# Performance work log

Measured on AMD Instinct MI355X. Metric: run time of the kernel, lower is better.

## Reference

```python
import jax, jax.numpy as jnp
import numpy as np

N = 10000   # nodes
E = 50000   # edges
C = 64      # in_channels / hidden
OUT = 64    # final out_channels


def _conv(x, src, dst, edge_attr, nn_w, nn_b, lin_w, bias):
    # edge MLP -> per-edge weight matrix [E, C, C]
    W = (edge_attr @ nn_w + nn_b).reshape(-1, C, C)
    x_j = x[src]                                   # gather source features [E, C]
    msg = jnp.einsum('ei,eio->eo', x_j, W)         # batched matvec [E, C]
    out = jax.ops.segment_sum(msg, dst, num_segments=N)  # scatter-add to targets
    out = out + x @ lin_w + bias                   # root weight + bias
    return out


def setup_inputs() -> dict:
    key = jax.random.key(0)
    ks = jax.random.split(key, 13)
    s = 1.0 / np.sqrt(C).astype(np.float32)
    return {
        'feature': jax.random.normal(ks[0], (N, C), dtype=jnp.float32),
        'edge_index': jax.random.randint(ks[1], (2, E), 0, N),
        'edge_attr': jax.random.normal(ks[2], (E, C), dtype=jnp.float32),
        # conv layer 0 (in=64 -> out=64)
        'nn_w0': jax.random.normal(ks[3], (C, C * C), dtype=jnp.float32) * s,
        'nn_b0': jnp.zeros((C * C,), dtype=jnp.float32),
        'lin_w0': jax.random.normal(ks[4], (C, C), dtype=jnp.float32) * s,
        'bias0': jnp.zeros((C,), dtype=jnp.float32),
        # conv layer 1 (64 -> 64)
        'nn_w1': jax.random.normal(ks[5], (C, C * C), dtype=jnp.float32) * s,
        'nn_b1': jnp.zeros((C * C,), dtype=jnp.float32),
        'lin_w1': jax.random.normal(ks[6], (C, C), dtype=jnp.float32) * s,
        'bias1': jnp.zeros((C,), dtype=jnp.float32),
        # final linear 64 -> 64
        'fin_w': jax.random.normal(ks[7], (C, OUT), dtype=jnp.float32) * s,
        'fin_b': jnp.zeros((OUT,), dtype=jnp.float32),
    }


def reference(feature, edge_index, edge_attr,
              nn_w0, nn_b0, lin_w0, bias0,
              nn_w1, nn_b1, lin_w1, bias1,
              fin_w, fin_b):
    src, dst = edge_index[0], edge_index[1]  # PyG flow: source_to_target
    x = jax.nn.relu(_conv(feature, src, dst, edge_attr, nn_w0, nn_b0, lin_w0, bias0))
    x = jax.nn.relu(_conv(x, src, dst, edge_attr, nn_w1, nn_b1, lin_w1, bias1))
    return x @ fin_w + fin_b
```

## Files before the change

### kernel.cpp

```cpp
#include <hip/hip_runtime.h>


#define NNODES 10000
#define NEDGES 50000
#define CH 64
#define NSTAGES 65
#define MW 64

typedef _Float16 f16;
typedef f16 f16x8 __attribute__((ext_vector_type(8)));
typedef float f32x4 __attribute__((ext_vector_type(4)));


__global__ void zero_kernel(int* __restrict__ hist, int* __restrict__ cursor) {
    int idx = blockIdx.x * 256 + threadIdx.x;
    if (idx < NNODES) { hist[idx] = 0; cursor[idx] = 0; }
}

__global__ void hist_kernel(const int* __restrict__ ei, int* __restrict__ hist) {
    int e = blockIdx.x * 256 + threadIdx.x;
    if (e < NEDGES) atomicAdd(&hist[ei[NEDGES + e]], 1);
}

__global__ __launch_bounds__(1024)
void scan_kernel(const int* __restrict__ hist, int* __restrict__ start) {
    __shared__ int buf[1024];
    int t = threadIdx.x;
    int base = t * 10;
    int loc[10];
    int s = 0;
#pragma unroll
    for (int i = 0; i < 10; ++i) {
        int n = base + i;
        int v = (n < NNODES) ? hist[n] : 0;
        loc[i] = s; s += v;
    }
    buf[t] = s;
    __syncthreads();
    for (int off = 1; off < 1024; off <<= 1) {
        int add = (t >= off) ? buf[t - off] : 0;
        __syncthreads();
        buf[t] += add;
        __syncthreads();
    }
    int ebase = buf[t] - s;
#pragma unroll
    for (int i = 0; i < 10; ++i) {
        int n = base + i;
        if (n < NNODES) start[n] = ebase + loc[i];
    }
    if (t == 1023) start[NNODES] = buf[1023];
}

__global__ void perm_kernel(const int* __restrict__ ei,
                            const int* __restrict__ start,
                            int* __restrict__ cursor,
                            int* __restrict__ eperm,
                            int* __restrict__ esrc) {
    int e = blockIdx.x * 256 + threadIdx.x;
    if (e < NEDGES) {
        int d = ei[NEDGES + e];
        int pos = start[d] + atomicAdd(&cursor[d], 1);
        eperm[pos] = e;
        esrc[pos]  = ei[e];
    }
}

__global__ void eagather_kernel(const float* __restrict__ ea,
                                const int* __restrict__ eperm,
                                float* __restrict__ eas) {
    int idx = blockIdx.x * 256 + threadIdx.x;
    if (idx >= NEDGES * 16) return;
    int p = idx >> 4, quad = idx & 15;
    int e = eperm[p];
    *(float4*)(eas + (size_t)p * 64 + quad * 4) =
        *(const float4*)(ea + (size_t)e * 64 + quad * 4);
}

__global__ void pack_b_kernel(const float* __restrict__ nw0, const float* __restrict__ nb0,
                              const float* __restrict__ nw1, const float* __restrict__ nb1,
                              f16* __restrict__ Bp0, f16* __restrict__ Bp1) {
    int idx = blockIdx.x * 256 + threadIdx.x;
    if (idx >= 2 * NSTAGES * 2048) return;
    int layer = (idx >= NSTAGES * 2048) ? 1 : 0;
    int r = idx - layer * NSTAGES * 2048;
    const float* nn_w = layer ? nw1 : nw0;
    const float* nn_b = layer ? nb1 : nb0;
    f16* Bp = layer ? Bp1 : Bp0;
    int p  = r & 3;
    int f  = r >> 2;
    int ln = f & 63;
    int q2 = (f >> 6) & 7;
    int s  = f >> 9;
    int tn = q2 >> 1, h = q2 & 1;
    int col  = tn * 16 + (ln & 15);
    int koff = h * 32 + (ln >> 4) * 8 + p * 2;
    float v0, v1;
    if (s < 64) {
        v0 = nn_w[(size_t)koff * 4096 + s * 64 + col];
        v1 = nn_w[(size_t)(koff + 1) * 4096 + s * 64 + col];
    } else {
        v0 = nn_b[koff * 64 + col];
        v1 = nn_b[(koff + 1) * 64 + col];
    }
    union { f16 h2[2]; unsigned u; } pk;
    pk.h2[0] = (f16)v0; pk.h2[1] = (f16)v1;
    *(unsigned*)((char*)Bp + (size_t)f * 16 + p * 4) = pk.u;
}

template<bool RELU_IN>
__global__ __launch_bounds__(64, 2)
void edge_gemm_kernel(const float* __restrict__ x,
                      const int* __restrict__ esrc,
                      const float* __restrict__ eas,
                      const f16* __restrict__ Bp,
                      float* __restrict__ msg) {
    __shared__ f16 xjS[MW][72];

    int ln  = threadIdx.x;
    int l15 = ln & 15, l4 = ln >> 4;
    int e0  = blockIdx.x * MW;
    int nh  = blockIdx.y;

#pragma unroll
    for (int r = 0; r < 16; ++r) {
        int idx = r * 64 + ln;
        int el = idx >> 4, ip = idx & 15;
        int p  = e0 + el;
        float4 v = {0.f, 0.f, 0.f, 0.f};
        if (p < NEDGES)
            v = *(const float4*)(x + (size_t)esrc[p] * CH + ip * 4);
        if (RELU_IN) {
            v.x = fmaxf(v.x, 0.f); v.y = fmaxf(v.y, 0.f);
            v.z = fmaxf(v.z, 0.f); v.w = fmaxf(v.w, 0.f);
        }
        union { f16 h4[4]; uint2 u; } pk;
        pk.h4[0] = (f16)v.x; pk.h4[1] = (f16)v.y;
        pk.h4[2] = (f16)v.z; pk.h4[3] = (f16)v.w;
        *(uint2*)&xjS[el][ip * 4] = pk.u;
    }

    f16x8 eav[4][2];
#pragma unroll
    for (int ms = 0; ms < 4; ++ms) {
        int p = e0 + ms * 16 + l15;
#pragma unroll
        for (int h = 0; h < 2; ++h) {
            float4 a = {0.f,0.f,0.f,0.f}, b = {0.f,0.f,0.f,0.f};
            if (p < NEDGES) {
                const float4* q = (const float4*)(eas + (size_t)p * CH + h * 32 + l4 * 8);
                a = q[0]; b = q[1];
            }
            f16x8 f;
            f[0]=(f16)a.x; f[1]=(f16)a.y; f[2]=(f16)a.z; f[3]=(f16)a.w;
            f[4]=(f16)b.x; f[5]=(f16)b.y; f[6]=(f16)b.z; f[7]=(f16)b.w;
            eav[ms][h] = f;
        }
    }

    f32x4 acc[4][2];
#pragma unroll
    for (int ms = 0; ms < 4; ++ms)
#pragma unroll
        for (int tl = 0; tl < 2; ++tl)
            acc[ms][tl] = (f32x4){0.f, 0.f, 0.f, 0.f};

    const char* gB = (const char*)Bp + nh * 4096 + ln * 16;

#define LOADB(b, sidx) do {                                                     \
        const char* _p = gB + (size_t)(sidx) * 8192;                            \
        b[0] = *(const f16x8*)(_p);                                             \
        b[1] = *(const f16x8*)(_p + 1024);                                      \
        b[2] = *(const f16x8*)(_p + 2048);                                      \
        b[3] = *(const f16x8*)(_p + 3072);                                      \
    } while (0)

#define COMP(sidx, b) do {                                                      \
        _Pragma("unroll")                                                       \
        for (int ms = 0; ms < 4; ++ms) {                                        \
            f16 xv = xjS[ms * 16 + l15][(sidx)];                                \
            f16x8 xsp = {xv, xv, xv, xv, xv, xv, xv, xv};                       \
            f16x8 a0 = eav[ms][0] * xsp;                                        \
            f16x8 a1 = eav[ms][1] * xsp;                                        \
            _Pragma("unroll")                                                   \
            for (int tl = 0; tl < 2; ++tl) {                                    \
                acc[ms][tl] = __builtin_amdgcn_mfma_f32_16x16x32_f16(a0, b[tl*2+0], acc[ms][tl], 0, 0, 0); \
                acc[ms][tl] = __builtin_amdgcn_mfma_f32_16x16x32_f16(a1, b[tl*2+1], acc[ms][tl], 0, 0, 0); \
            }                                                                   \
        }                                                                       \
    } while (0)

#define WAIT8 do { asm volatile("s_waitcnt vmcnt(8)" ::: "memory");             \
                   __builtin_amdgcn_sched_barrier(0); } while (0)

    f16x8 b0[4], b1[4], b2[4];
    LOADB(b0, 0); LOADB(b1, 1); LOADB(b2, 2);
    asm volatile("s_waitcnt vmcnt(0)" ::: "memory");
    __builtin_amdgcn_sched_barrier(0);

#pragma unroll 1
    for (int s = 0; s < 63; s += 3) {
        WAIT8; COMP(s,     b0); LOADB(b0, s + 3);
        WAIT8; COMP(s + 1, b1); LOADB(b1, s + 4);
        WAIT8; COMP(s + 2, b2); LOADB(b2, min(s + 5, 64));
    }
    WAIT8;
    COMP(63, b0);
    asm volatile("s_waitcnt vmcnt(4)" ::: "memory");
    __builtin_amdgcn_sched_barrier(0);
#pragma unroll
    for (int ms = 0; ms < 4; ++ms)
#pragma unroll
        for (int h = 0; h < 2; ++h) {
            f16x8 af = *(const f16x8*)&xjS[ms * 16 + l15][h * 32 + l4 * 8];
#pragma unroll
            for (int tl = 0; tl < 2; ++tl)
                acc[ms][tl] = __builtin_amdgcn_mfma_f32_16x16x32_f16(af, b1[tl * 2 + h], acc[ms][tl], 0, 0, 0);
        }

#pragma unroll
    for (int ms = 0; ms < 4; ++ms)
#pragma unroll
        for (int q = 0; q < 4; ++q) {
            int p = e0 + ms * 16 + l4 * 4 + q;
            if (p < NEDGES) {
                float* row = msg + (size_t)p * CH + nh * 32;
                row[l15]      = acc[ms][0][q];
                row[16 + l15] = acc[ms][1][q];
            }
        }
#undef LOADB
#undef COMP
#undef WAIT8
}

template<bool RELU_IN>
__global__ __launch_bounds__(256)
void rootreduce_kernel(const float* __restrict__ x,
                       const float* __restrict__ lw,
                       const float* __restrict__ bias,
                       const float* __restrict__ msg,
                       const int* __restrict__ start,
                       float* __restrict__ outb) {
    int o  = threadIdx.x & 63;
    int gw = (blockIdx.x * 256 + threadIdx.x) >> 6;
    float lwc[64];
#pragma unroll
    for (int k = 0; k < 64; ++k) lwc[k] = lw[k * 64 + o];
    float bo = bias[o];
    for (int n = gw; n < NNODES; n += 1024) {
        const float4* xr = (const float4*)(x + (size_t)n * 64);
        float acc = bo;
#pragma unroll
        for (int kq = 0; kq < 16; ++kq) {
            float4 xv = xr[kq];
            float a = xv.x, b = xv.y, c = xv.z, d = xv.w;
            if (RELU_IN) {
                a = fmaxf(a, 0.f); b = fmaxf(b, 0.f);
                c = fmaxf(c, 0.f); d = fmaxf(d, 0.f);
            }
            acc = fmaf(a, lwc[kq * 4 + 0], acc);
            acc = fmaf(b, lwc[kq * 4 + 1], acc);
            acc = fmaf(c, lwc[kq * 4 + 2], acc);
            acc = fmaf(d, lwc[kq * 4 + 3], acc);
        }
        int pb = start[n], pe = start[n + 1];
        int p = pb;
        for (; p + 4 <= pe; p += 4) {
            float v0 = msg[(size_t)(p + 0) * 64 + o];
            float v1 = msg[(size_t)(p + 1) * 64 + o];
            float v2 = msg[(size_t)(p + 2) * 64 + o];
            float v3 = msg[(size_t)(p + 3) * 64 + o];
            acc += (v0 + v1) + (v2 + v3);
        }
        for (; p < pe; ++p)
            acc += msg[(size_t)p * 64 + o];
        outb[(size_t)n * 64 + o] = acc;
    }
}

__global__ __launch_bounds__(256)
void final_kernel(const float* __restrict__ x,
                  const float* __restrict__ fw,
                  const float* __restrict__ fb,
                  float* __restrict__ out) {
    int o  = threadIdx.x & 63;
    int gw = (blockIdx.x * 256 + threadIdx.x) >> 6;
    float fwc[64];
#pragma unroll
    for (int k = 0; k < 64; ++k) fwc[k] = fw[k * 64 + o];
    float bo = fb[o];
    for (int n = gw; n < NNODES; n += 1024) {
        const float4* xr = (const float4*)(x + (size_t)n * 64);
        float acc = bo;
#pragma unroll
        for (int kq = 0; kq < 16; ++kq) {
            float4 xv = xr[kq];
            acc = fmaf(fmaxf(xv.x, 0.f), fwc[kq * 4 + 0], acc);
            acc = fmaf(fmaxf(xv.y, 0.f), fwc[kq * 4 + 1], acc);
            acc = fmaf(fmaxf(xv.z, 0.f), fwc[kq * 4 + 2], acc);
            acc = fmaf(fmaxf(xv.w, 0.f), fwc[kq * 4 + 3], acc);
        }
        out[(size_t)n * 64 + o] = acc;
    }
}

extern "C" void kernel_launch(void* const* d_in, const int* in_sizes, int n_in,
                              void* d_out, int out_size, void* d_ws, size_t ws_size,
                              hipStream_t stream) {
    const float* feature = (const float*)d_in[0];
    const int*   ei      = (const int*)d_in[1];
    const float* ea      = (const float*)d_in[2];
    const float* nn_w0   = (const float*)d_in[3];
    const float* nn_b0   = (const float*)d_in[4];
    const float* lin_w0  = (const float*)d_in[5];
    const float* bias0   = (const float*)d_in[6];
    const float* nn_w1   = (const float*)d_in[7];
    const float* nn_b1   = (const float*)d_in[8];
    const float* lin_w1  = (const float*)d_in[9];
    const float* bias1   = (const float*)d_in[10];
    const float* fin_w   = (const float*)d_in[11];
    const float* fin_b   = (const float*)d_in[12];
    float* out = (float*)d_out;

    char* ws = (char*)d_ws;
    float* buf0   = (float*)(ws + 0);
    float* buf1   = (float*)(ws + 2560000);
    f16*   Bp0    = (f16*)  (ws + 5120000);
    f16*   Bp1    = (f16*)  (ws + 5652480);
    int*   hist   = (int*)  (ws + 6184960);
    int*   cursor = (int*)  (ws + 6224960);
    int*   startp = (int*)  (ws + 6264960);
    int*   eperm  = (int*)  (ws + 6304976);
    int*   esrc   = (int*)  (ws + 6504976);
    float* eas    = (float*)(ws + 6704976);
    float* msg    = (float*)(ws + 19504976);

    zero_kernel<<<(NNODES + 255) / 256, 256, 0, stream>>>(hist, cursor);
    hist_kernel<<<(NEDGES + 255) / 256, 256, 0, stream>>>(ei, hist);
    scan_kernel<<<1, 1024, 0, stream>>>(hist, startp);
    perm_kernel<<<(NEDGES + 255) / 256, 256, 0, stream>>>(ei, startp, cursor, eperm, esrc);
    eagather_kernel<<<(NEDGES * 16 + 255) / 256, 256, 0, stream>>>(ea, eperm, eas);

    pack_b_kernel<<<(2 * NSTAGES * 2048 + 255) / 256, 256, 0, stream>>>(
        nn_w0, nn_b0, nn_w1, nn_b1, Bp0, Bp1);

    dim3 eg((NEDGES + MW - 1) / MW, 2);

    edge_gemm_kernel<false><<<eg, 64, 0, stream>>>(feature, esrc, eas, Bp0, msg);
    rootreduce_kernel<false><<<256, 256, 0, stream>>>(feature, lin_w0, bias0,
                                                      msg, startp, buf0);
    edge_gemm_kernel<true><<<eg, 64, 0, stream>>>(buf0, esrc, eas, Bp1, msg);
    rootreduce_kernel<true><<<256, 256, 0, stream>>>(buf0, lin_w1, bias1,
                                                     msg, startp, buf1);
    final_kernel<<<256, 256, 0, stream>>>(buf1, fin_w, fin_b, out);
}
```

Before: 174.6 us.

## Stage B tiles through LDS with async global_load_lds ring and fuse final linear

The edge GEMM now streams the packed per-edge weight tiles into a 6-deep LDS ring using global_load_lds instead of holding triple-buffered register copies, and drops the 2-waves-per-SIMD launch bound. The final linear layer is fused into the second root/reduce kernel through a per-wave shared row, which removes one launch and one intermediate buffer round trip. The zero kernel is replaced by memset calls. The LDS ring adds about 24KB of shared memory per block, which may lower occupancy. The LDS reads in COMP rely only on vmcnt waits with no barrier, which is safe only because each block is a single wave.

```diff
diff --git a/kernel.cpp b/kernel.cpp
--- a/kernel.cpp
+++ b/kernel.cpp
@@ -11,11 +11,10 @@
 typedef f16 f16x8 __attribute__((ext_vector_type(8)));
 typedef float f32x4 __attribute__((ext_vector_type(4)));
 
-
-__global__ void zero_kernel(int* __restrict__ hist, int* __restrict__ cursor) {
-    int idx = blockIdx.x * 256 + threadIdx.x;
-    if (idx < NNODES) { hist[idx] = 0; cursor[idx] = 0; }
-}
+#define GLOAD_LDS16(gptr, lptr) __builtin_amdgcn_global_load_lds(               \
+        (const __attribute__((address_space(1))) void*)(gptr),                  \
+        (__attribute__((address_space(3))) void*)(lptr), 16, 0, 0)
+
 
 __global__ void hist_kernel(const int* __restrict__ ei, int* __restrict__ hist) {
     int e = blockIdx.x * 256 + threadIdx.x;
@@ -109,13 +108,14 @@
 }
 
 template<bool RELU_IN>
-__global__ __launch_bounds__(64, 2)
+__global__ __launch_bounds__(64)
 void edge_gemm_kernel(const float* __restrict__ x,
                       const int* __restrict__ esrc,
                       const float* __restrict__ eas,
                       const f16* __restrict__ Bp,
                       float* __restrict__ msg) {
     __shared__ f16 xjS[MW][72];
+    __shared__ __align__(16) f16 BS[6][2048];
 
     int ln  = threadIdx.x;
     int l15 = ln & 15, l4 = ln >> 4;
@@ -167,56 +167,69 @@
 
     const char* gB = (const char*)Bp + nh * 4096 + ln * 16;
 
-#define LOADB(b, sidx) do {                                                     \
-        const char* _p = gB + (size_t)(sidx) * 8192;                            \
-        b[0] = *(const f16x8*)(_p);                                             \
-        b[1] = *(const f16x8*)(_p + 1024);                                      \
-        b[2] = *(const f16x8*)(_p + 2048);                                      \
-        b[3] = *(const f16x8*)(_p + 3072);                                      \
+#define STAGE(ring, sidx) do {                                                  \
+        const char* _g = gB + (size_t)(sidx) * 8192;                            \
+        char* _l = (char*)&BS[(ring)][0];                                       \
+        GLOAD_LDS16(_g,        _l);                                             \
+        GLOAD_LDS16(_g + 1024, _l + 1024);                                      \
+        GLOAD_LDS16(_g + 2048, _l + 2048);                                      \
+        GLOAD_LDS16(_g + 3072, _l + 3072);                                      \
     } while (0)
 
-#define COMP(sidx, b) do {                                                      \
+#define COMP(sidx, ring) do {                                                   \
+        f16x8 bf0 = *(const f16x8*)&BS[(ring)][ln * 8];                         \
+        f16x8 bf1 = *(const f16x8*)&BS[(ring)][512 + ln * 8];                   \
+        f16x8 bf2 = *(const f16x8*)&BS[(ring)][1024 + ln * 8];                  \
+        f16x8 bf3 = *(const f16x8*)&BS[(ring)][1536 + ln * 8];                  \
         _Pragma("unroll")                                                       \
         for (int ms = 0; ms < 4; ++ms) {                                        \
             f16 xv = xjS[ms * 16 + l15][(sidx)];                                \
             f16x8 xsp = {xv, xv, xv, xv, xv, xv, xv, xv};                       \
             f16x8 a0 = eav[ms][0] * xsp;                                        \
             f16x8 a1 = eav[ms][1] * xsp;                                        \
-            _Pragma("unroll")                                                   \
-            for (int tl = 0; tl < 2; ++tl) {                                    \
-                acc[ms][tl] = __builtin_amdgcn_mfma_f32_16x16x32_f16(a0, b[tl*2+0], acc[ms][tl], 0, 0, 0); \
-                acc[ms][tl] = __builtin_amdgcn_mfma_f32_16x16x32_f16(a1, b[tl*2+1], acc[ms][tl], 0, 0, 0); \
-            }                                                                   \
+            acc[ms][0] = __builtin_amdgcn_mfma_f32_16x16x32_f16(a0, bf0, acc[ms][0], 0, 0, 0); \
+            acc[ms][0] = __builtin_amdgcn_mfma_f32_16x16x32_f16(a1, bf1, acc[ms][0], 0, 0, 0); \
+            acc[ms][1] = __builtin_amdgcn_mfma_f32_16x16x32_f16(a0, bf2, acc[ms][1], 0, 0, 0); \
+            acc[ms][1] = __builtin_amdgcn_mfma_f32_16x16x32_f16(a1, bf3, acc[ms][1], 0, 0, 0); \
         }                                                                       \
     } while (0)
 
-#define WAIT8 do { asm volatile("s_waitcnt vmcnt(8)" ::: "memory");             \
-                   __builtin_amdgcn_sched_barrier(0); } while (0)
-
-    f16x8 b0[4], b1[4], b2[4];
-    LOADB(b0, 0); LOADB(b1, 1); LOADB(b2, 2);
+#define VWAIT(n) do { asm volatile("s_waitcnt vmcnt(" #n ")" ::: "memory");     \
+                      __builtin_amdgcn_sched_barrier(0); } while (0)
+
     asm volatile("s_waitcnt vmcnt(0)" ::: "memory");
     __builtin_amdgcn_sched_barrier(0);
+    STAGE(0, 0); STAGE(1, 1); STAGE(2, 2); STAGE(3, 3); STAGE(4, 4);
 
 #pragma unroll 1
-    for (int s = 0; s < 63; s += 3) {
-        WAIT8; COMP(s,     b0); LOADB(b0, s + 3);
-        WAIT8; COMP(s + 1, b1); LOADB(b1, s + 4);
-        WAIT8; COMP(s + 2, b2); LOADB(b2, min(s + 5, 64));
-    }
-    WAIT8;
-    COMP(63, b0);
-    asm volatile("s_waitcnt vmcnt(4)" ::: "memory");
-    __builtin_amdgcn_sched_barrier(0);
-#pragma unroll
-    for (int ms = 0; ms < 4; ++ms)
-#pragma unroll
-        for (int h = 0; h < 2; ++h) {
-            f16x8 af = *(const f16x8*)&xjS[ms * 16 + l15][h * 32 + l4 * 8];
-#pragma unroll
-            for (int tl = 0; tl < 2; ++tl)
-                acc[ms][tl] = __builtin_amdgcn_mfma_f32_16x16x32_f16(af, b1[tl * 2 + h], acc[ms][tl], 0, 0, 0);
-        }
+    for (int s = 0; s < 60; s += 6) {
+        VWAIT(16); COMP(s + 0, 0); STAGE(5, s + 5);
+        VWAIT(16); COMP(s + 1, 1); STAGE(0, s + 6);
+        VWAIT(16); COMP(s + 2, 2); STAGE(1, s + 7);
+        VWAIT(16); COMP(s + 3, 3); STAGE(2, s + 8);
+        VWAIT(16); COMP(s + 4, 4); STAGE(3, s + 9);
+        VWAIT(16); COMP(s + 5, 5); STAGE(4, s + 10);
+    }
+    VWAIT(16); COMP(60, 0);
+    VWAIT(12); COMP(61, 1);
+    VWAIT(8);  COMP(62, 2);
+    VWAIT(4);  COMP(63, 3);
+    VWAIT(0);
+    {
+        f16x8 bf0 = *(const f16x8*)&BS[4][ln * 8];
+        f16x8 bf1 = *(const f16x8*)&BS[4][512 + ln * 8];
+        f16x8 bf2 = *(const f16x8*)&BS[4][1024 + ln * 8];
+        f16x8 bf3 = *(const f16x8*)&BS[4][1536 + ln * 8];
+#pragma unroll
+        for (int ms = 0; ms < 4; ++ms) {
+            f16x8 af0 = *(const f16x8*)&xjS[ms * 16 + l15][l4 * 8];
+            f16x8 af1 = *(const f16x8*)&xjS[ms * 16 + l15][32 + l4 * 8];
+            acc[ms][0] = __builtin_amdgcn_mfma_f32_16x16x32_f16(af0, bf0, acc[ms][0], 0, 0, 0);
+            acc[ms][0] = __builtin_amdgcn_mfma_f32_16x16x32_f16(af1, bf1, acc[ms][0], 0, 0, 0);
+            acc[ms][1] = __builtin_amdgcn_mfma_f32_16x16x32_f16(af0, bf2, acc[ms][1], 0, 0, 0);
+            acc[ms][1] = __builtin_amdgcn_mfma_f32_16x16x32_f16(af1, bf3, acc[ms][1], 0, 0, 0);
+        }
+    }
 
 #pragma unroll
     for (int ms = 0; ms < 4; ++ms)
@@ -229,24 +242,35 @@
                 row[16 + l15] = acc[ms][1][q];
             }
         }
-#undef LOADB
+#undef STAGE
 #undef COMP
-#undef WAIT8
-}
-
-template<bool RELU_IN>
+#undef VWAIT
+}
+
+template<bool RELU_IN, bool FINAL>
 __global__ __launch_bounds__(256)
 void rootreduce_kernel(const float* __restrict__ x,
                        const float* __restrict__ lw,
                        const float* __restrict__ bias,
                        const float* __restrict__ msg,
                        const int* __restrict__ start,
+                       const float* __restrict__ fw,
+                       const float* __restrict__ fb,
                        float* __restrict__ outb) {
+    __shared__ float vrow[4][64];
     int o  = threadIdx.x & 63;
+    int wv = threadIdx.x >> 6;
     int gw = (blockIdx.x * 256 + threadIdx.x) >> 6;
     float lwc[64];
 #pragma unroll
     for (int k = 0; k < 64; ++k) lwc[k] = lw[k * 64 + o];
+    float fwc[64];
+    float fbo = 0.f;
+    if (FINAL) {
+#pragma unroll
+        for (int k = 0; k < 64; ++k) fwc[k] = fw[k * 64 + o];
+        fbo = fb[o];
+    }
     float bo = bias[o];
     for (int n = gw; n < NNODES; n += 1024) {
         const float4* xr = (const float4*)(x + (size_t)n * 64);
@@ -275,33 +299,16 @@
         }
         for (; p < pe; ++p)
             acc += msg[(size_t)p * 64 + o];
-        outb[(size_t)n * 64 + o] = acc;
-    }
-}
-
-__global__ __launch_bounds__(256)
-void final_kernel(const float* __restrict__ x,
-                  const float* __restrict__ fw,
-                  const float* __restrict__ fb,
-                  float* __restrict__ out) {
-    int o  = threadIdx.x & 63;
-    int gw = (blockIdx.x * 256 + threadIdx.x) >> 6;
-    float fwc[64];
-#pragma unroll
-    for (int k = 0; k < 64; ++k) fwc[k] = fw[k * 64 + o];
-    float bo = fb[o];
-    for (int n = gw; n < NNODES; n += 1024) {
-        const float4* xr = (const float4*)(x + (size_t)n * 64);
-        float acc = bo;
-#pragma unroll
-        for (int kq = 0; kq < 16; ++kq) {
-            float4 xv = xr[kq];
-            acc = fmaf(fmaxf(xv.x, 0.f), fwc[kq * 4 + 0], acc);
-            acc = fmaf(fmaxf(xv.y, 0.f), fwc[kq * 4 + 1], acc);
-            acc = fmaf(fmaxf(xv.z, 0.f), fwc[kq * 4 + 2], acc);
-            acc = fmaf(fmaxf(xv.w, 0.f), fwc[kq * 4 + 3], acc);
-        }
-        out[(size_t)n * 64 + o] = acc;
+        if (FINAL) {
+            vrow[wv][o] = fmaxf(acc, 0.f);
+            float a2 = fbo;
+#pragma unroll
+            for (int k = 0; k < 64; ++k)
+                a2 = fmaf(vrow[wv][k], fwc[k], a2);
+            outb[(size_t)n * 64 + o] = a2;
+        } else {
+            outb[(size_t)n * 64 + o] = acc;
+        }
     }
 }
 
@@ -325,18 +332,18 @@
 
     char* ws = (char*)d_ws;
     float* buf0   = (float*)(ws + 0);
-    float* buf1   = (float*)(ws + 2560000);
-    f16*   Bp0    = (f16*)  (ws + 5120000);
-    f16*   Bp1    = (f16*)  (ws + 5652480);
-    int*   hist   = (int*)  (ws + 6184960);
-    int*   cursor = (int*)  (ws + 6224960);
-    int*   startp = (int*)  (ws + 6264960);
-    int*   eperm  = (int*)  (ws + 6304976);
-    int*   esrc   = (int*)  (ws + 6504976);
-    float* eas    = (float*)(ws + 6704976);
-    float* msg    = (float*)(ws + 19504976);
-
-    zero_kernel<<<(NNODES + 255) / 256, 256, 0, stream>>>(hist, cursor);
+    f16*   Bp0    = (f16*)  (ws + 2560000);
+    f16*   Bp1    = (f16*)  (ws + 3092480);
+    int*   hist   = (int*)  (ws + 3624960);
+    int*   cursor = (int*)  (ws + 3664960);
+    int*   startp = (int*)  (ws + 3704960);
+    int*   eperm  = (int*)  (ws + 3744976);
+    int*   esrc   = (int*)  (ws + 3944976);
+    float* eas    = (float*)(ws + 4144976);
+    float* msg    = (float*)(ws + 16944976);
+
+    hipMemsetAsync(hist, 0, NNODES * sizeof(int), stream);
+    hipMemsetAsync(cursor, 0, NNODES * sizeof(int), stream);
     hist_kernel<<<(NEDGES + 255) / 256, 256, 0, stream>>>(ei, hist);
     scan_kernel<<<1, 1024, 0, stream>>>(hist, startp);
     perm_kernel<<<(NEDGES + 255) / 256, 256, 0, stream>>>(ei, startp, cursor, eperm, esrc);
@@ -348,10 +355,9 @@
     dim3 eg((NEDGES + MW - 1) / MW, 2);
 
     edge_gemm_kernel<false><<<eg, 64, 0, stream>>>(feature, esrc, eas, Bp0, msg);
-    rootreduce_kernel<false><<<256, 256, 0, stream>>>(feature, lin_w0, bias0,
-                                                      msg, startp, buf0);
+    rootreduce_kernel<false, false><<<256, 256, 0, stream>>>(
+        feature, lin_w0, bias0, msg, startp, fin_w, fin_b, buf0);
     edge_gemm_kernel<true><<<eg, 64, 0, stream>>>(buf0, esrc, eas, Bp1, msg);
-    rootreduce_kernel<true><<<256, 256, 0, stream>>>(buf0, lin_w1, bias1,
-                                                     msg, startp, buf1);
-    final_kernel<<<256, 256, 0, stream>>>(buf1, fin_w, fin_b, out);
-}
+    rootreduce_kernel<true, true><<<256, 256, 0, stream>>>(
+        buf0, lin_w1, bias1, msg, startp, fin_w, fin_b, out);
+}
```

Measured after the change: 206.8 us. 1.18x slower.
